# Performance work log

Hardware: AMD Instinct MI355X
Metric: run time of the kernel (lower is better)

## Reference

```python
import jax, jax.numpy as jnp
import numpy as np

TAU = 1.0  # temperaturesa
GRID = 5   # torch.chunk(..., 5) along H and W


def _cam(X, gamma, tau):
    # Channel attention: energy = Xf Xf^T over spatial dim, with max-subtraction/negation trick.
    B, C, H, W = X.shape
    Xf = X.reshape(B, C, H * W)
    energy = jnp.einsum('bcn,bdn->bcd', Xf, Xf)                      # [B,C,C]
    energy_new = jnp.max(energy, axis=-1, keepdims=True) - energy
    attn = jax.nn.softmax(energy_new / tau, axis=-1)
    out = jnp.einsum('bcd,bdn->bcn', attn, Xf).reshape(B, C, H, W)
    return gamma * out + X


def _pam(X, Wq, bq, Wk, bk, Wv, bv, gamma, tau):
    # Position attention with 1x1-conv q/k/v (1x1 conv == channel matmul).
    B, C, H, W = X.shape
    N = H * W
    Xf = X.reshape(B, C, N)
    q = jnp.einsum('kc,bcn->bnk', Wq, Xf) + bq                        # [B,N,C//8]
    k = jnp.einsum('kc,bcn->bkn', Wk, Xf) + bk[None, :, None]         # [B,C//8,N]
    v = jnp.einsum('dc,bcn->bdn', Wv, Xf) + bv[None, :, None]         # [B,C,N]
    energy = jnp.einsum('bnk,bkm->bnm', q, k)                         # [B,N,N]
    attn = jax.nn.softmax(energy / tau, axis=-1)
    # torch: bmm(value, attention.permute(0,2,1)) -> out[b,d,m] = sum_n v[b,d,n]*attn[b,m,n]
    out = jnp.einsum('bdn,bmn->bdm', v, attn).reshape(B, C, H, W)
    return gamma * out + X


def _cka_loss(X, Y):
    # linear_CKA_loss: HKH centering done as K - rowmean - colmean + totalmean.
    def cgram(Z):
        K = Z @ Z.T                                                   # [B,B]
        rm = jnp.mean(K, axis=1, keepdims=True)
        cm = jnp.mean(K, axis=0, keepdims=True)
        return K - rm - cm + jnp.mean(K)
    cX, cY = cgram(X), cgram(Y)
    hsic = jnp.sum(cX * cY)
    v1 = jnp.sqrt(jnp.sum(cX * cX))
    v2 = jnp.sqrt(jnp.sum(cY * cY))
    return -jnp.log(jnp.abs(hsic / (v1 * v2)) + 1e-8)


def _grid_chunks(X, g=GRID):
    # 5x5 spatial tiling -> [g*g, B, C, H/g, W/g]
    B, C, H, W = X.shape
    h, w = H // g, W // g
    return X.reshape(B, C, g, h, g, w).transpose(2, 4, 0, 1, 3, 5).reshape(g * g, B, C, h, w)


def setup_inputs() -> dict:
    key = jax.random.key(0)
    ks = jax.random.split(key, 10)
    B, C, H, W = 16, 256, 80, 80
    Ck = C // 8
    return {
        'feat_S': jax.random.normal(ks[0], (B, C, H, W), jnp.float32),
        'feat_T': jax.random.normal(ks[1], (B, C, H, W), jnp.float32),
        'Wq': jax.random.normal(ks[2], (Ck, C), jnp.float32),
        'bq': jax.random.normal(ks[3], (Ck,), jnp.float32),
        'Wk': jax.random.normal(ks[4], (Ck, C), jnp.float32),
        'bk': jax.random.normal(ks[5], (Ck,), jnp.float32),
        'Wv': jax.random.normal(ks[6], (C, C), jnp.float32),
        'bv': jax.random.normal(ks[7], (C,), jnp.float32),
        'gammacam': jax.random.normal(ks[8], (1,), jnp.float32),
        'gammapam': jax.random.normal(ks[9], (1,), jnp.float32),
    }


def reference(feat_S, feat_T, Wq, bq, Wk, bk, Wv, bv, gammacam, gammapam):
    # feature_transform == 'separately_CAMgridPAM_CKA'
    tau = TAU
    pam = lambda X: _pam(X, Wq, bq, Wk, bk, Wv, bv, gammapam, tau)
    chunks_S = _grid_chunks(feat_S)                                   # [25,B,C,16,16]
    chunks_T = _grid_chunks(feat_T)
    pam_S = jax.vmap(pam)(chunks_S)
    pam_T = jax.vmap(pam)(chunks_T)
    nchunk, B = pam_S.shape[0], pam_S.shape[1]
    flat_S = pam_S.reshape(nchunk, B, -1)
    flat_T = pam_T.reshape(nchunk, B, -1)
    loss_PAM = jnp.mean(jax.vmap(_cka_loss)(flat_S, flat_T))          # sum/n == mean
    CAM_S = _cam(feat_S, gammacam, tau)
    CAM_T = _cam(feat_T, gammacam, tau)
    loss_CAM = _cka_loss(CAM_S.reshape(B, -1), CAM_T.reshape(B, -1))
    return (loss_CAM, loss_PAM)
```

## Files before the change

### kernel.cpp

```cpp
#include <hip/hip_runtime.h>


typedef short bf16x8 __attribute__((ext_vector_type(8)));
typedef float f32x4 __attribute__((ext_vector_type(4)));

constexpr int BB = 16;
constexpr int CH = 256;
constexpr int HW = 6400;
constexpr int IMW = 80;

__device__ __forceinline__ int lds_off(int row, int half, int k2) {
  return row * 128 + ((((half << 6)) | k2) ^ ((row & 7) << 4));
}

__device__ __forceinline__ bf16x8 frag_ld(const char* base, int row, int half, int lane) {
  int off = row * 128 + ((((half << 6)) | ((lane >> 4) << 4)) ^ ((lane & 7) << 4));
  return *(const bf16x8*)(base + off);
}

__device__ __forceinline__ void cvt2(float x, unsigned short& h, unsigned short& l) {
  unsigned u = __float_as_uint(x);
  h = (unsigned short)(u >> 16);
  float r = x - __uint_as_float(u & 0xffff0000u);
  l = (unsigned short)(__float_as_uint(r) >> 16);
}

__device__ __forceinline__ void cvt4(float4 v, ushort4& h, ushort4& l) {
  cvt2(v.x, h.x, l.x); cvt2(v.y, h.y, l.y);
  cvt2(v.z, h.z, l.z); cvt2(v.w, h.w, l.w);
}

__device__ __forceinline__ void cvt8(float4 v0, float4 v1, bf16x8& hi, bf16x8& lo) {
  unsigned short h, l;
  cvt2(v0.x, h, l); hi[0] = (short)h; lo[0] = (short)l;
  cvt2(v0.y, h, l); hi[1] = (short)h; lo[1] = (short)l;
  cvt2(v0.z, h, l); hi[2] = (short)h; lo[2] = (short)l;
  cvt2(v0.w, h, l); hi[3] = (short)h; lo[3] = (short)l;
  cvt2(v1.x, h, l); hi[4] = (short)h; lo[4] = (short)l;
  cvt2(v1.y, h, l); hi[5] = (short)h; lo[5] = (short)l;
  cvt2(v1.z, h, l); hi[6] = (short)h; lo[6] = (short)l;
  cvt2(v1.w, h, l); hi[7] = (short)h; lo[7] = (short)l;
}

__device__ __forceinline__ unsigned short bf_rnd(float x) {
  unsigned u = __float_as_uint(x);
  return (unsigned short)((u + 0x8000u) >> 16);
}

__global__ __launch_bounds__(512) void cam_energy_k(const float* __restrict__ fS,
                                                    const float* __restrict__ fT,
                                                    float* __restrict__ part) {
  const int kc = blockIdx.x, b = blockIdx.y, t = blockIdx.z;
  const float* X = (t ? fT : fS) + (size_t)b * CH * HW;
  __shared__ unsigned short lds[256 * 64];
  char* Ab = (char*)lds;
  const int tid = threadIdx.x, lane = tid & 63, w = tid >> 6;
  const int wr = w >> 2, wc = w & 3;
  const int r0 = tid >> 1, half = tid & 1;
  const float* Xr = X + (size_t)r0 * HW + kc * 640 + half * 32;
  f32x4 acc[8][4] = {};
  float4 v[8];
#pragma unroll
  for (int q = 0; q < 8; ++q) v[q] = *(const float4*)(Xr + q * 4);
  for (int it = 0; it < 10; ++it) {
    __syncthreads();
#pragma unroll
    for (int q = 0; q < 8; ++q) {
      ushort4 u;
      u.x = bf_rnd(v[q].x); u.y = bf_rnd(v[q].y);
      u.z = bf_rnd(v[q].z); u.w = bf_rnd(v[q].w);
      *(ushort4*)(Ab + lds_off(r0, half, q * 8)) = u;
    }
    __syncthreads();
    float4 nv[8];
    if (it < 9) {
      const float* Xn = Xr + (it + 1) * 64;
#pragma unroll
      for (int q = 0; q < 8; ++q) nv[q] = *(const float4*)(Xn + q * 4);
    }
    bf16x8 bfr[2][4];
#pragma unroll
    for (int h = 0; h < 2; ++h)
#pragma unroll
      for (int n = 0; n < 4; ++n)
        bfr[h][n] = frag_ld(Ab, wc * 64 + n * 16 + (lane & 15), h, lane);
#pragma unroll
    for (int m = 0; m < 8; ++m) {
      int arow = wr * 128 + m * 16 + (lane & 15);
      bf16x8 a0 = frag_ld(Ab, arow, 0, lane);
      bf16x8 a1 = frag_ld(Ab, arow, 1, lane);
#pragma unroll
      for (int n = 0; n < 4; ++n)
        acc[m][n] = __builtin_amdgcn_mfma_f32_16x16x32_bf16(a0, bfr[0][n], acc[m][n], 0, 0, 0);
#pragma unroll
      for (int n = 0; n < 4; ++n)
        acc[m][n] = __builtin_amdgcn_mfma_f32_16x16x32_bf16(a1, bfr[1][n], acc[m][n], 0, 0, 0);
    }
#pragma unroll
    for (int q = 0; q < 8; ++q) v[q] = nv[q];
  }
  float* Eb = part + (((size_t)kc * 2 + t) * BB + b) * 65536;
#pragma unroll
  for (int m = 0; m < 8; ++m)
#pragma unroll
    for (int n = 0; n < 4; ++n) {
      int row = wr * 128 + m * 16 + ((lane >> 4) << 2);
      int col = wc * 64 + n * 16 + (lane & 15);
#pragma unroll
      for (int r2 = 0; r2 < 4; ++r2)
        Eb[(size_t)(row + r2) * 256 + col] = acc[m][n][r2];
    }
}

__global__ __launch_bounds__(64) void cam_softmax_k(float* __restrict__ part) {
  const int c = blockIdx.x, b = blockIdx.y, t = blockIdx.z;
  const size_t base = (((size_t)t * BB + b) * CH + c) * CH;
  const int lane = threadIdx.x;
  float4 x = make_float4(0.f, 0.f, 0.f, 0.f);
#pragma unroll
  for (int p = 0; p < 10; ++p) {
    float4 y = ((const float4*)(part + (size_t)p * 2097152 + base))[lane];
    x.x += y.x; x.y += y.y; x.z += y.z; x.w += y.w;
  }
  float mn = fminf(fminf(x.x, x.y), fminf(x.z, x.w));
  for (int o = 32; o; o >>= 1) mn = fminf(mn, __shfl_xor(mn, o));
  float4 p4;
  p4.x = __expf(mn - x.x); p4.y = __expf(mn - x.y);
  p4.z = __expf(mn - x.z); p4.w = __expf(mn - x.w);
  float s = (p4.x + p4.y) + (p4.z + p4.w);
  for (int o = 32; o; o >>= 1) s += __shfl_xor(s, o);
  const float inv = 1.0f / s;
  p4.x *= inv; p4.y *= inv; p4.z *= inv; p4.w *= inv;
  ((float4*)(part + base))[lane] = p4;
}

template <int MODE>
__global__ __launch_bounds__(256) void ax_k(const float* __restrict__ Abase, int Astride,
                                            const float* __restrict__ X,
                                            float* __restrict__ OUT,
                                            const float* __restrict__ bvec,
                                            const float* __restrict__ gsc) {
  const int mt = blockIdx.x / 50, nt = blockIdx.x % 50;
  const int b = blockIdx.y;
  const float* A = Abase + (size_t)b * Astride;
  const float* Xb = X + (size_t)b * CH * HW;
  float* OUTb = OUT + (size_t)b * CH * HW;
  const int nbase = nt * 128;
  __shared__ unsigned short lds[2 * 128 * 64];
  char* Ab = (char*)lds;
  char* Bb = (char*)lds + 16384;
  const int tid = threadIdx.x, lane = tid & 63, w = tid >> 6;
  const int wr = w >> 1, wc = w & 1;
  const int r0 = tid >> 3, kq = tid & 7;
  const int n4 = (tid & 31) * 4, c0l = tid >> 5;
  f32x4 acc[4][4] = {};
  float4 ra[4], rb[4];
#pragma unroll
  for (int q = 0; q < 4; ++q) {
    ra[q] = *(const float4*)(A + (size_t)(mt * 128 + r0 + 32 * q) * 256 + kq * 4);
    rb[q] = *(const float4*)(Xb + (size_t)(c0l + 8 * q) * HW + nbase + n4);
  }
  for (int s = 0; s < 8; ++s) {
#pragma unroll
    for (int q = 0; q < 4; ++q) {
      int rr = r0 + 32 * q;
      ushort4 h4, l4;
      cvt4(ra[q], h4, l4);
      *(ushort4*)(Ab + lds_off(rr, 0, kq * 8)) = h4;
      *(ushort4*)(Ab + lds_off(rr, 1, kq * 8)) = l4;
    }
#pragma unroll
    for (int q = 0; q < 4; ++q) {
      int cc = c0l + 8 * q;
      float4 v = rb[q];
#pragma unroll
      for (int jj = 0; jj < 4; ++jj) {
        int j = (jj + tid) & 3;
        float e = (j == 0) ? v.x : (j == 1) ? v.y : (j == 2) ? v.z : v.w;
        unsigned short h, l;
        cvt2(e, h, l);
        int row = n4 + j;
        *(unsigned short*)(Bb + lds_off(row, 0, cc * 2)) = h;
        *(unsigned short*)(Bb + lds_off(row, 1, cc * 2)) = l;
      }
    }
    __syncthreads();
    if (s < 7) {
      int k0 = (s + 1) * 32;
#pragma unroll
      for (int q = 0; q < 4; ++q) {
        ra[q] = *(const float4*)(A + (size_t)(mt * 128 + r0 + 32 * q) * 256 + k0 + kq * 4);
        rb[q] = *(const float4*)(Xb + (size_t)(k0 + c0l + 8 * q) * HW + nbase + n4);
      }
    }
    bf16x8 bfr[2][4];
#pragma unroll
    for (int h = 0; h < 2; ++h)
#pragma unroll
      for (int n = 0; n < 4; ++n)
        bfr[h][n] = frag_ld(Bb, wc * 64 + n * 16 + (lane & 15), h, lane);
#pragma unroll
    for (int m = 0; m < 4; ++m) {
      int arow = wr * 64 + m * 16 + (lane & 15);
      bf16x8 a0 = frag_ld(Ab, arow, 0, lane);
      bf16x8 a1 = frag_ld(Ab, arow, 1, lane);
#pragma unroll
      for (int n = 0; n < 4; ++n)
        acc[m][n] = __builtin_amdgcn_mfma_f32_16x16x32_bf16(a0, bfr[0][n], acc[m][n], 0, 0, 0);
#pragma unroll
      for (int n = 0; n < 4; ++n)
        acc[m][n] = __builtin_amdgcn_mfma_f32_16x16x32_bf16(a0, bfr[1][n], acc[m][n], 0, 0, 0);
#pragma unroll
      for (int n = 0; n < 4; ++n)
        acc[m][n] = __builtin_amdgcn_mfma_f32_16x16x32_bf16(a1, bfr[0][n], acc[m][n], 0, 0, 0);
    }
    __syncthreads();
  }
  float g = 0.f;
  if (MODE == 0) g = gsc[0];
#pragma unroll
  for (int m = 0; m < 4; ++m)
#pragma unroll
    for (int n = 0; n < 4; ++n) {
      int row = mt * 128 + wr * 64 + m * 16 + ((lane >> 4) << 2);
      int col = nbase + wc * 64 + n * 16 + (lane & 15);
#pragma unroll
      for (int r2 = 0; r2 < 4; ++r2) {
        size_t o = (size_t)(row + r2) * HW + col;
        float v = acc[m][n][r2];
        if (MODE == 0) OUTb[o] = g * v + Xb[o];
        else           OUTb[o] = v + bvec[row + r2];
      }
    }
}

__global__ __launch_bounds__(256) void qk_k(const float* __restrict__ X,
                                            const float* __restrict__ Wq,
                                            const float* __restrict__ bq,
                                            const float* __restrict__ Wk,
                                            const float* __restrict__ bk,
                                            float* __restrict__ qt,
                                            float* __restrict__ kf) {
  const int nbase = blockIdx.x * 256;
  const int b = blockIdx.y;
  const float* Xb = X + (size_t)b * CH * HW;
  __shared__ unsigned short lds[(64 + 256) * 64];
  char* Ab = (char*)lds;
  char* Bb = (char*)lds + 8192;
  const int tid = threadIdx.x, lane = tid & 63, w = tid >> 6;
  const int ar = tid >> 2, akq = tid & 3;
  const int n4 = (tid & 63) * 4, c0l = tid >> 6;
  const float* Arow = (ar < 32) ? (Wq + (size_t)ar * CH) : (Wk + (size_t)(ar - 32) * CH);
  f32x4 acc[4][4] = {};
  float4 va[2], vb[8];
#pragma unroll
  for (int q = 0; q < 2; ++q)
    va[q] = *(const float4*)(Arow + akq * 8 + q * 4);
#pragma unroll
  for (int q = 0; q < 8; ++q)
    vb[q] = *(const float4*)(Xb + (size_t)(c0l + 4 * q) * HW + nbase + n4);
  for (int s = 0; s < 8; ++s) {
    __syncthreads();
#pragma unroll
    for (int q = 0; q < 2; ++q) {
      ushort4 h4, l4;
      cvt4(va[q], h4, l4);
      *(ushort4*)(Ab + lds_off(ar, 0, akq * 16 + q * 8)) = h4;
      *(ushort4*)(Ab + lds_off(ar, 1, akq * 16 + q * 8)) = l4;
    }
#pragma unroll
    for (int q = 0; q < 8; ++q) {
      int cc = c0l + 4 * q;
      float4 v = vb[q];
#pragma unroll
      for (int jj = 0; jj < 4; ++jj) {
        int j = (jj + tid) & 3;
        float e = (j == 0) ? v.x : (j == 1) ? v.y : (j == 2) ? v.z : v.w;
        unsigned short h, l;
        cvt2(e, h, l);
        int row = n4 + j;
        *(unsigned short*)(Bb + lds_off(row, 0, cc * 2)) = h;
        *(unsigned short*)(Bb + lds_off(row, 1, cc * 2)) = l;
      }
    }
    __syncthreads();
    float4 na[2], nb[8];
    if (s < 7) {
      const int k0 = (s + 1) * 32;
#pragma unroll
      for (int q = 0; q < 2; ++q)
        na[q] = *(const float4*)(Arow + k0 + akq * 8 + q * 4);
#pragma unroll
      for (int q = 0; q < 8; ++q)
        nb[q] = *(const float4*)(Xb + (size_t)(k0 + c0l + 4 * q) * HW + nbase + n4);
    }
    bf16x8 bfr[2][4];
#pragma unroll
    for (int h = 0; h < 2; ++h)
#pragma unroll
      for (int n = 0; n < 4; ++n)
        bfr[h][n] = frag_ld(Bb, w * 64 + n * 16 + (lane & 15), h, lane);
#pragma unroll
    for (int m = 0; m < 4; ++m) {
      int arow2 = m * 16 + (lane & 15);
      bf16x8 a0 = frag_ld(Ab, arow2, 0, lane);
      bf16x8 a1 = frag_ld(Ab, arow2, 1, lane);
#pragma unroll
      for (int n = 0; n < 4; ++n)
        acc[m][n] = __builtin_amdgcn_mfma_f32_16x16x32_bf16(a0, bfr[0][n], acc[m][n], 0, 0, 0);
#pragma unroll
      for (int n = 0; n < 4; ++n)
        acc[m][n] = __builtin_amdgcn_mfma_f32_16x16x32_bf16(a0, bfr[1][n], acc[m][n], 0, 0, 0);
#pragma unroll
      for (int n = 0; n < 4; ++n)
        acc[m][n] = __builtin_amdgcn_mfma_f32_16x16x32_bf16(a1, bfr[0][n], acc[m][n], 0, 0, 0);
    }
#pragma unroll
    for (int q = 0; q < 2; ++q) va[q] = na[q];
#pragma unroll
    for (int q = 0; q < 8; ++q) vb[q] = nb[q];
  }
#pragma unroll
  for (int m = 0; m < 4; ++m)
#pragma unroll
    for (int n = 0; n < 4; ++n) {
      int row = m * 16 + ((lane >> 4) << 2);
      int col = nbase + w * 64 + n * 16 + (lane & 15);
#pragma unroll
      for (int r2 = 0; r2 < 4; ++r2) {
        int rr = row + r2;
        float v = acc[m][n][r2];
        if (rr < 32) qt[((size_t)b * HW + col) * 32 + rr] = v + bq[rr];
        else         kf[((size_t)b * 32 + (rr - 32)) * HW + col] = v + bk[rr - 32];
      }
    }
}

__global__ __launch_bounds__(256) void pam_es_k(const float* __restrict__ qt,
                                                const float* __restrict__ kf,
                                                float* __restrict__ Pbuf) {
  const int ccb = blockIdx.x;
  const int ck = ccb >> 4, b = ccb & 15;
  const int gi = ck / 5, gj = ck % 5;
  const int pbase = gi * 16 * IMW + gj * 16;
  float* Pc = Pbuf + (size_t)ccb * 65536;
  __shared__ float qs[256][32];
  __shared__ float S[32][256];
  const int tid = threadIdx.x;
  const float* qb = qt + (size_t)b * HW * 32;
#pragma unroll
  for (int qq = 0; qq < 8; ++qq) {
    int j = (tid >> 3) + 32 * qq;
    int nj = pbase + (j >> 4) * IMW + (j & 15);
    float4 v = *(const float4*)(qb + (size_t)nj * 32 + (tid & 7) * 4);
    *(float4*)&qs[j][(tid & 7) * 4] = v;
  }
  const int nt = pbase + (tid >> 4) * IMW + (tid & 15);
  const float* kb = kf + (size_t)b * 32 * HW;
  float kc[32];
#pragma unroll
  for (int kk = 0; kk < 32; ++kk) kc[kk] = kb[(size_t)kk * HW + nt];
  __syncthreads();
  const int w = tid >> 6, lane = tid & 63;
  for (int p = 0; p < 8; ++p) {
#pragma unroll 4
    for (int j2 = 0; j2 < 32; ++j2) {
      int row = p * 32 + j2;
      float s = 0.f;
#pragma unroll
      for (int k8 = 0; k8 < 8; ++k8) {
        float4 qv = *(const float4*)&qs[row][k8 * 4];
        s = fmaf(qv.x, kc[k8 * 4 + 0], s);
        s = fmaf(qv.y, kc[k8 * 4 + 1], s);
        s = fmaf(qv.z, kc[k8 * 4 + 2], s);
        s = fmaf(qv.w, kc[k8 * 4 + 3], s);
      }
      S[j2][tid] = s;
    }
    __syncthreads();
#pragma unroll
    for (int rr = 0; rr < 8; ++rr) {
      int jj = w * 8 + rr;
      float4 v = *(const float4*)&S[jj][lane << 2];
      float m = fmaxf(fmaxf(v.x, v.y), fmaxf(v.z, v.w));
      for (int o = 32; o; o >>= 1) m = fmaxf(m, __shfl_xor(m, o));
      float4 pv;
      pv.x = __expf(v.x - m); pv.y = __expf(v.y - m);
      pv.z = __expf(v.z - m); pv.w = __expf(v.w - m);
      float s = (pv.x + pv.y) + (pv.z + pv.w);
      for (int o = 32; o; o >>= 1) s += __shfl_xor(s, o);
      const float inv = 1.f / s;
      pv.x *= inv; pv.y *= inv; pv.z *= inv; pv.w *= inv;
      *(float4*)&Pc[(size_t)(p * 32 + jj) * 256 + (lane << 2)] = pv;
    }
    __syncthreads();
  }
}

__global__ __launch_bounds__(512) void pam_pv_k(float* __restrict__ P,
                                                const float* __restrict__ V,
                                                const float* __restrict__ fS,
                                                const float* __restrict__ fT,
                                                const float* __restrict__ gsc, int t) {
  const int ccb = blockIdx.x;
  const int ck = ccb >> 4, b = ccb & 15;
  const int gi = ck / 5, gj = ck % 5;
  const float* Xb = (t ? fT : fS) + (size_t)b * CH * HW;
  const float* Vb = V + (size_t)b * CH * HW;
  float* Pc = P + (size_t)ccb * 65536;
  __shared__ unsigned short lds[2 * 256 * 64];
  char* Ab = (char*)lds;
  char* Bb = (char*)lds + 32768;
  const int tid = threadIdx.x, lane = tid & 63, w = tid >> 6;
  const int wr = w >> 2, wc = w & 3;
  const int r0 = tid >> 3, kq = tid & 7;
  const int pbase = gi * 16 * IMW + gj * 16;
  f32x4 acc[8][4] = {};
  float4 va[4], vb[4];
  {
    int jj = kq * 4;
    int ngl = pbase + (jj >> 4) * IMW + (jj & 15);
#pragma unroll
    for (int q = 0; q < 4; ++q) {
      int rr = r0 + 64 * q;
      va[q] = *(const float4*)(Vb + (size_t)rr * HW + ngl);
      vb[q] = *(const float4*)(Pc + (size_t)rr * 256 + kq * 4);
    }
  }
  for (int s = 0; s < 8; ++s) {
    __syncthreads();
#pragma unroll
    for (int q = 0; q < 4; ++q) {
      int rr = r0 + 64 * q;
      ushort4 h4, l4;
      cvt4(va[q], h4, l4);
      *(ushort4*)(Ab + lds_off(rr, 0, kq * 8)) = h4;
      *(ushort4*)(Ab + lds_off(rr, 1, kq * 8)) = l4;
      cvt4(vb[q], h4, l4);
      *(ushort4*)(Bb + lds_off(rr, 0, kq * 8)) = h4;
      *(ushort4*)(Bb + lds_off(rr, 1, kq * 8)) = l4;
    }
    __syncthreads();
    float4 na[4], nb[4];
    if (s < 7) {
      int k0 = (s + 1) * 32;
      int jj = k0 + kq * 4;
      int ngl = pbase + (jj >> 4) * IMW + (jj & 15);
#pragma unroll
      for (int q = 0; q < 4; ++q) {
        int rr = r0 + 64 * q;
        na[q] = *(const float4*)(Vb + (size_t)rr * HW + ngl);
        nb[q] = *(const float4*)(Pc + (size_t)rr * 256 + k0 + kq * 4);
      }
    }
    bf16x8 bfr[2][4];
#pragma unroll
    for (int h = 0; h < 2; ++h)
#pragma unroll
      for (int n = 0; n < 4; ++n)
        bfr[h][n] = frag_ld(Bb, wc * 64 + n * 16 + (lane & 15), h, lane);
#pragma unroll
    for (int m = 0; m < 8; ++m) {
      int arow = wr * 128 + m * 16 + (lane & 15);
      bf16x8 a0 = frag_ld(Ab, arow, 0, lane);
      bf16x8 a1 = frag_ld(Ab, arow, 1, lane);
#pragma unroll
      for (int n = 0; n < 4; ++n)
        acc[m][n] = __builtin_amdgcn_mfma_f32_16x16x32_bf16(a0, bfr[0][n], acc[m][n], 0, 0, 0);
#pragma unroll
      for (int n = 0; n < 4; ++n)
        acc[m][n] = __builtin_amdgcn_mfma_f32_16x16x32_bf16(a0, bfr[1][n], acc[m][n], 0, 0, 0);
#pragma unroll
      for (int n = 0; n < 4; ++n)
        acc[m][n] = __builtin_amdgcn_mfma_f32_16x16x32_bf16(a1, bfr[0][n], acc[m][n], 0, 0, 0);
    }
#pragma unroll
    for (int q = 0; q < 4; ++q) { va[q] = na[q]; vb[q] = nb[q]; }
  }
  const float g = gsc[0];
#pragma unroll
  for (int m = 0; m < 8; ++m)
#pragma unroll
    for (int n = 0; n < 4; ++n) {
      int row = wr * 128 + m * 16 + ((lane >> 4) << 2);
      int col = wc * 64 + n * 16 + (lane & 15);
      int ngl = pbase + (col >> 4) * IMW + (col & 15);
#pragma unroll
      for (int r2 = 0; r2 < 4; ++r2) {
        float v = g * acc[m][n][r2] + Xb[(size_t)(row + r2) * HW + ngl];
        Pc[(size_t)(row + r2) * 256 + col] = v;
      }
    }
}

__global__ __launch_bounds__(256) void gram_mfma_k(const float* __restrict__ Z,
                                                   size_t gStride, size_t bStride,
                                                   double* __restrict__ G) {
  const int tid = threadIdx.x, lane = tid & 63, w = tid >> 6;
  const float* Zg = Z + (size_t)blockIdx.y * gStride;
  const float* p = Zg + (size_t)(lane & 15) * bStride +
                   (size_t)blockIdx.x * 4096 + w * 1024 + ((lane >> 4) << 3);
  f32x4 acc = {};
#pragma unroll 4
  for (int s = 0; s < 32; ++s) {
    float4 v0 = *(const float4*)(p + s * 32);
    float4 v1 = *(const float4*)(p + s * 32 + 4);
    bf16x8 hi, lo;
    cvt8(v0, v1, hi, lo);
    acc = __builtin_amdgcn_mfma_f32_16x16x32_bf16(hi, hi, acc, 0, 0, 0);
    acc = __builtin_amdgcn_mfma_f32_16x16x32_bf16(hi, lo, acc, 0, 0, 0);
    acc = __builtin_amdgcn_mfma_f32_16x16x32_bf16(lo, hi, acc, 0, 0, 0);
  }
  double* Gt = G + (size_t)blockIdx.y * 256;
  const int col = lane & 15, row0 = (lane >> 4) << 2;
#pragma unroll
  for (int i = 0; i < 4; ++i)
    atomicAdd(&Gt[(size_t)(row0 + i) * 16 + col], (double)acc[i]);
}

__global__ __launch_bounds__(256) void cka_pair_k(const double* __restrict__ G,
                                                  double* __restrict__ losses) {
  const int q = blockIdx.x;
  const double* KX = (q == 0) ? G : G + 512 + (size_t)(q - 1) * 256;
  const double* KY = (q == 0) ? G + 256 : G + 512 + 6400 + (size_t)(q - 1) * 256;
  __shared__ double red[256];
  __shared__ double srm[16], scm[16];
  __shared__ double stm;
  const int tid = threadIdx.x;
  const int r = tid >> 4, c = tid & 15;

  auto center = [&](double k) -> double {
    red[tid] = k;
    __syncthreads();
    for (int off = 8; off; off >>= 1) {
      if (c < off) red[tid] += red[tid + off];
      __syncthreads();
    }
    if (c == 0) srm[r] = red[tid] * (1.0 / 16.0);
    __syncthreads();
    red[c * 16 + r] = k;
    __syncthreads();
    for (int off = 8; off; off >>= 1) {
      if (r < off) red[c * 16 + r] += red[c * 16 + r + off];
      __syncthreads();
    }
    if (r == 0) scm[c] = red[c * 16] * (1.0 / 16.0);
    __syncthreads();
    if (tid == 0) {
      double s = 0.0;
      for (int i = 0; i < 16; ++i) s += srm[i];
      stm = s * (1.0 / 16.0);
    }
    __syncthreads();
    double v = k - srm[r] - scm[c] + stm;
    __syncthreads();
    return v;
  };
  auto reduce_sum = [&](double v) -> double {
    red[tid] = v;
    __syncthreads();
    for (int off = 128; off; off >>= 1) {
      if (tid < off) red[tid] += red[tid + off];
      __syncthreads();
    }
    double s = red[0];
    __syncthreads();
    return s;
  };
  double cx = center(KX[tid]);
  double cy = center(KY[tid]);
  double h = reduce_sum(cx * cy);
  double v1 = reduce_sum(cx * cx);
  double v2 = reduce_sum(cy * cy);
  if (tid == 0) losses[q] = -log(fabs(h / (sqrt(v1) * sqrt(v2))) + 1e-8);
}

__global__ void cka_combine_k(const double* __restrict__ losses,
                              float* __restrict__ out) {
  if (threadIdx.x == 0) {
    out[0] = (float)losses[0];
    double s = 0.0;
    for (int q = 1; q <= 25; ++q) s += losses[q];
    out[1] = (float)(s * (1.0 / 25.0));
  }
}

extern "C" void kernel_launch(void* const* d_in, const int* in_sizes, int n_in,
                              void* d_out, int out_size, void* d_ws, size_t ws_size,
                              hipStream_t stream) {
  (void)in_sizes; (void)n_in; (void)out_size; (void)ws_size;
  const float* fS = (const float*)d_in[0];
  const float* fT = (const float*)d_in[1];
  const float* Wq = (const float*)d_in[2];
  const float* bq = (const float*)d_in[3];
  const float* Wk = (const float*)d_in[4];
  const float* bk = (const float*)d_in[5];
  const float* Wv = (const float*)d_in[6];
  const float* bv = (const float*)d_in[7];
  const float* gcam = (const float*)d_in[8];
  const float* gpam = (const float*)d_in[9];
  float* out = (float*)d_out;

  float* buf0 = (float*)d_ws;
  float* buf1 = buf0 + 26214400;
  double* G = (double*)(buf1 + 26214400);
  float* Pbuf = buf1;
  float* qt = buf0;
  float* kf = buf0 + 3276800;
  double* losses = (double*)buf0;

  hipMemsetAsync(G, 0, 13312 * sizeof(double), stream);

  cam_energy_k<<<dim3(10, 16, 2), 512, 0, stream>>>(fS, fT, buf1);
  cam_softmax_k<<<dim3(256, 16, 2), 64, 0, stream>>>(buf1);
  for (int t = 0; t < 2; ++t) {
    ax_k<0><<<dim3(100, 16), 256, 0, stream>>>(buf1 + (size_t)t * BB * 65536, 65536,
                                               t ? fT : fS, buf0, nullptr, gcam);
    gram_mfma_k<<<dim3(400, 1), 256, 0, stream>>>(buf0, (size_t)0, (size_t)1638400,
                                                  G + t * 256);
  }
  for (int t = 0; t < 2; ++t) {
    const float* X = t ? fT : fS;
    qk_k<<<dim3(25, 16), 256, 0, stream>>>(X, Wq, bq, Wk, bk, qt, kf);
    pam_es_k<<<dim3(400), 256, 0, stream>>>(qt, kf, Pbuf);
    ax_k<1><<<dim3(100, 16), 256, 0, stream>>>(Wv, 0, X, buf0, bv, nullptr);
    pam_pv_k<<<dim3(400), 512, 0, stream>>>(Pbuf, buf0, fS, fT, gpam, t);
    gram_mfma_k<<<dim3(16, 25), 256, 0, stream>>>(Pbuf, (size_t)1048576, (size_t)65536,
                                                  G + 512 + t * 6400);
  }
  cka_pair_k<<<dim3(26), 256, 0, stream>>>(G, losses);
  cka_combine_k<<<dim3(1), 64, 0, stream>>>(losses, out);
}
```

Measured before the change: 1.105 ms.

## Double-buffer CAM energy LDS, cut split-K partials, widen ax_k tiles

The CAM energy kernel now double-buffers its LDS tile, which drops one barrier per iteration, and splits K into 8 chunks of 800 instead of 10 of 640. The tail chunk is zero-padded, and the softmax kernel sums 8 partial buffers instead of 10. ax_k now uses 512-thread blocks that cover all 256 output rows per N tile, so each X tile is loaded and converted once instead of twice. In exchange ax_k uses more LDS and registers per block, and launches fewer, larger blocks for both kernels.

```diff
diff --git a/kernel.cpp b/kernel.cpp
--- a/kernel.cpp
+++ b/kernel.cpp
@@ -52,43 +52,49 @@
                                                     float* __restrict__ part) {
   const int kc = blockIdx.x, b = blockIdx.y, t = blockIdx.z;
   const float* X = (t ? fT : fS) + (size_t)b * CH * HW;
-  __shared__ unsigned short lds[256 * 64];
-  char* Ab = (char*)lds;
+  __shared__ unsigned short lds[2 * 256 * 64];
   const int tid = threadIdx.x, lane = tid & 63, w = tid >> 6;
   const int wr = w >> 2, wc = w & 3;
   const int r0 = tid >> 1, half = tid & 1;
-  const float* Xr = X + (size_t)r0 * HW + kc * 640 + half * 32;
+  const int kbase = kc * 800 + half * 32;
+  const float* Xr = X + (size_t)r0 * HW + kbase;
   f32x4 acc[8][4] = {};
   float4 v[8];
 #pragma unroll
   for (int q = 0; q < 8; ++q) v[q] = *(const float4*)(Xr + q * 4);
-  for (int it = 0; it < 10; ++it) {
-    __syncthreads();
+  for (int it = 0; it < 13; ++it) {
+    char* pb = (char*)lds + (it & 1) * 32768;
 #pragma unroll
     for (int q = 0; q < 8; ++q) {
       ushort4 u;
       u.x = bf_rnd(v[q].x); u.y = bf_rnd(v[q].y);
       u.z = bf_rnd(v[q].z); u.w = bf_rnd(v[q].w);
-      *(ushort4*)(Ab + lds_off(r0, half, q * 8)) = u;
+      *(ushort4*)(pb + lds_off(r0, half, q * 8)) = u;
     }
     __syncthreads();
     float4 nv[8];
-    if (it < 9) {
-      const float* Xn = Xr + (it + 1) * 64;
-#pragma unroll
-      for (int q = 0; q < 8; ++q) nv[q] = *(const float4*)(Xn + q * 4);
+    if (it < 12) {
+      const int nk = (it + 1) * 64;
+      if (nk + half * 32 < 800) {
+        const float* Xn = Xr + nk;
+#pragma unroll
+        for (int q = 0; q < 8; ++q) nv[q] = *(const float4*)(Xn + q * 4);
+      } else {
+#pragma unroll
+        for (int q = 0; q < 8; ++q) nv[q] = make_float4(0.f, 0.f, 0.f, 0.f);
+      }
     }
     bf16x8 bfr[2][4];
 #pragma unroll
     for (int h = 0; h < 2; ++h)
 #pragma unroll
       for (int n = 0; n < 4; ++n)
-        bfr[h][n] = frag_ld(Ab, wc * 64 + n * 16 + (lane & 15), h, lane);
+        bfr[h][n] = frag_ld(pb, wc * 64 + n * 16 + (lane & 15), h, lane);
 #pragma unroll
     for (int m = 0; m < 8; ++m) {
       int arow = wr * 128 + m * 16 + (lane & 15);
-      bf16x8 a0 = frag_ld(Ab, arow, 0, lane);
-      bf16x8 a1 = frag_ld(Ab, arow, 1, lane);
+      bf16x8 a0 = frag_ld(pb, arow, 0, lane);
+      bf16x8 a1 = frag_ld(pb, arow, 1, lane);
 #pragma unroll
       for (int n = 0; n < 4; ++n)
         acc[m][n] = __builtin_amdgcn_mfma_f32_16x16x32_bf16(a0, bfr[0][n], acc[m][n], 0, 0, 0);
@@ -118,7 +124,7 @@
   const int lane = threadIdx.x;
   float4 x = make_float4(0.f, 0.f, 0.f, 0.f);
 #pragma unroll
-  for (int p = 0; p < 10; ++p) {
+  for (int p = 0; p < 8; ++p) {
     float4 y = ((const float4*)(part + (size_t)p * 2097152 + base))[lane];
     x.x += y.x; x.y += y.y; x.z += y.z; x.w += y.w;
   }
@@ -135,43 +141,43 @@
 }
 
 template <int MODE>
-__global__ __launch_bounds__(256) void ax_k(const float* __restrict__ Abase, int Astride,
+__global__ __launch_bounds__(512) void ax_k(const float* __restrict__ Abase, int Astride,
                                             const float* __restrict__ X,
                                             float* __restrict__ OUT,
                                             const float* __restrict__ bvec,
                                             const float* __restrict__ gsc) {
-  const int mt = blockIdx.x / 50, nt = blockIdx.x % 50;
+  const int nt = blockIdx.x;
   const int b = blockIdx.y;
   const float* A = Abase + (size_t)b * Astride;
   const float* Xb = X + (size_t)b * CH * HW;
   float* OUTb = OUT + (size_t)b * CH * HW;
   const int nbase = nt * 128;
-  __shared__ unsigned short lds[2 * 128 * 64];
+  __shared__ unsigned short lds[(256 + 128) * 64];
   char* Ab = (char*)lds;
-  char* Bb = (char*)lds + 16384;
+  char* Bb = (char*)lds + 32768;
   const int tid = threadIdx.x, lane = tid & 63, w = tid >> 6;
   const int wr = w >> 1, wc = w & 1;
-  const int r0 = tid >> 3, kq = tid & 7;
+  const int r0 = tid >> 1, kq = tid & 1;
   const int n4 = (tid & 31) * 4, c0l = tid >> 5;
   f32x4 acc[4][4] = {};
-  float4 ra[4], rb[4];
-#pragma unroll
-  for (int q = 0; q < 4; ++q) {
-    ra[q] = *(const float4*)(A + (size_t)(mt * 128 + r0 + 32 * q) * 256 + kq * 4);
-    rb[q] = *(const float4*)(Xb + (size_t)(c0l + 8 * q) * HW + nbase + n4);
-  }
+  float4 ra[4], rb[2];
+#pragma unroll
+  for (int q = 0; q < 4; ++q)
+    ra[q] = *(const float4*)(A + (size_t)r0 * 256 + kq * 16 + q * 4);
+#pragma unroll
+  for (int q = 0; q < 2; ++q)
+    rb[q] = *(const float4*)(Xb + (size_t)(c0l + 16 * q) * HW + nbase + n4);
   for (int s = 0; s < 8; ++s) {
 #pragma unroll
     for (int q = 0; q < 4; ++q) {
-      int rr = r0 + 32 * q;
       ushort4 h4, l4;
       cvt4(ra[q], h4, l4);
-      *(ushort4*)(Ab + lds_off(rr, 0, kq * 8)) = h4;
-      *(ushort4*)(Ab + lds_off(rr, 1, kq * 8)) = l4;
-    }
-#pragma unroll
-    for (int q = 0; q < 4; ++q) {
-      int cc = c0l + 8 * q;
+      *(ushort4*)(Ab + lds_off(r0, 0, kq * 32 + q * 8)) = h4;
+      *(ushort4*)(Ab + lds_off(r0, 1, kq * 32 + q * 8)) = l4;
+    }
+#pragma unroll
+    for (int q = 0; q < 2; ++q) {
+      int cc = c0l + 16 * q;
       float4 v = rb[q];
 #pragma unroll
       for (int jj = 0; jj < 4; ++jj) {
@@ -188,10 +194,11 @@
     if (s < 7) {
       int k0 = (s + 1) * 32;
 #pragma unroll
-      for (int q = 0; q < 4; ++q) {
-        ra[q] = *(const float4*)(A + (size_t)(mt * 128 + r0 + 32 * q) * 256 + k0 + kq * 4);
-        rb[q] = *(const float4*)(Xb + (size_t)(k0 + c0l + 8 * q) * HW + nbase + n4);
-      }
+      for (int q = 0; q < 4; ++q)
+        ra[q] = *(const float4*)(A + (size_t)r0 * 256 + k0 + kq * 16 + q * 4);
+#pragma unroll
+      for (int q = 0; q < 2; ++q)
+        rb[q] = *(const float4*)(Xb + (size_t)(k0 + c0l + 16 * q) * HW + nbase + n4);
     }
     bf16x8 bfr[2][4];
 #pragma unroll
@@ -222,7 +229,7 @@
   for (int m = 0; m < 4; ++m)
 #pragma unroll
     for (int n = 0; n < 4; ++n) {
-      int row = mt * 128 + wr * 64 + m * 16 + ((lane >> 4) << 2);
+      int row = wr * 64 + m * 16 + ((lane >> 4) << 2);
       int col = nbase + wc * 64 + n * 16 + (lane & 15);
 #pragma unroll
       for (int r2 = 0; r2 < 4; ++r2) {
@@ -611,11 +618,11 @@
 
   hipMemsetAsync(G, 0, 13312 * sizeof(double), stream);
 
-  cam_energy_k<<<dim3(10, 16, 2), 512, 0, stream>>>(fS, fT, buf1);
+  cam_energy_k<<<dim3(8, 16, 2), 512, 0, stream>>>(fS, fT, buf1);
   cam_softmax_k<<<dim3(256, 16, 2), 64, 0, stream>>>(buf1);
   for (int t = 0; t < 2; ++t) {
-    ax_k<0><<<dim3(100, 16), 256, 0, stream>>>(buf1 + (size_t)t * BB * 65536, 65536,
-                                               t ? fT : fS, buf0, nullptr, gcam);
+    ax_k<0><<<dim3(50, 16), 512, 0, stream>>>(buf1 + (size_t)t * BB * 65536, 65536,
+                                              t ? fT : fS, buf0, nullptr, gcam);
     gram_mfma_k<<<dim3(400, 1), 256, 0, stream>>>(buf0, (size_t)0, (size_t)1638400,
                                                   G + t * 256);
   }
@@ -623,7 +630,7 @@
     const float* X = t ? fT : fS;
     qk_k<<<dim3(25, 16), 256, 0, stream>>>(X, Wq, bq, Wk, bk, qt, kf);
     pam_es_k<<<dim3(400), 256, 0, stream>>>(qt, kf, Pbuf);
-    ax_k<1><<<dim3(100, 16), 256, 0, stream>>>(Wv, 0, X, buf0, bv, nullptr);
+    ax_k<1><<<dim3(50, 16), 512, 0, stream>>>(Wv, 0, X, buf0, bv, nullptr);
     pam_pv_k<<<dim3(400), 512, 0, stream>>>(Pbuf, buf0, fS, fT, gpam, t);
     gram_mfma_k<<<dim3(16, 25), 256, 0, stream>>>(Pbuf, (size_t)1048576, (size_t)65536,
                                                   G + 512 + t * 6400);
```

New measurement: 1.072 ms. 1.03x faster.
